# Kernel tuning notes

Measured on AMD Instinct MI355X. Metric: run time of the kernel, lower is better.

The kernel has to match this reference:

```python
import jax, jax.numpy as jnp
import numpy as np

TOP_K = 2  # num_experts_per_tok


def setup_inputs() -> dict:
    key = jax.random.key(0)
    ks = jax.random.split(key, 5)
    B, T, D, E, F = 2, 2048, 1024, 8, 2048
    scale_d = 1.0 / np.sqrt(D)
    scale_f = 1.0 / np.sqrt(F)
    return {
        "x": jax.random.normal(ks[0], (B, T, D), jnp.float32),
        "kernel_router_DE": jax.random.normal(ks[1], (D, E), jnp.float32) * scale_d,
        "kernel_gating_EDF": jax.random.normal(ks[2], (E, D, F), jnp.float32) * scale_d,
        "kernel_up_EDF": jax.random.normal(ks[3], (E, D, F), jnp.float32) * scale_d,
        "kernel_down_EFD": jax.random.normal(ks[4], (E, F, D), jnp.float32) * scale_f,
    }


def reference(x, kernel_router_DE, kernel_gating_EDF, kernel_up_EDF, kernel_down_EFD):
    E = kernel_router_DE.shape[-1]
    x = x.astype(jnp.float32)

    # --- Router: logits -> softmax -> top_k -> renormalize with softmax ---
    router_logits_BTE = jnp.einsum('BTD,DE->BTE', x, kernel_router_DE)
    probs_BTE = jax.nn.softmax(router_logits_BTE.astype(jnp.float32), axis=-1)
    weights_BTX, indices_BTX = jax.lax.top_k(probs_BTE, TOP_K)
    norm_weights_BTX = jax.nn.softmax(weights_BTX, axis=-1)

    # --- Scatter top-k weights back to dense per-expert weights ---
    one_hot_BTXE = jax.nn.one_hot(indices_BTX, num_classes=E, dtype=jnp.float32)
    full_weights_BTE = jnp.sum(one_hot_BTXE * norm_weights_BTX[..., None], axis=2)

    # --- Dense all-expert MLP (gating * up -> down), weighted combine ---
    gating_BTEF = jnp.einsum('BTD,EDF->BTEF', x, kernel_gating_EDF)
    fuse_BTEF = jax.nn.silu(gating_BTEF) * jnp.einsum('BTD,EDF->BTEF', x, kernel_up_EDF)
    down_BTED = jnp.einsum('BTEF,EFD->BTED', fuse_BTEF, kernel_down_EFD)
    out_BTD = jnp.einsum('BTED,BTE->BTD', down_BTED, full_weights_BTE)
    return out_BTD.astype(jnp.float32)
```

## Files before the change

kernel.cpp:

```cpp
#include <hip/hip_runtime.h>
#include <cstdint>

#define N_TOK 4096
#define DIM   1024
#define NEXP  8
#define FDIM  2048

typedef _Float16 f16_t;
typedef _Float16 f16x8 __attribute__((ext_vector_type(8)));
typedef float    f32x4 __attribute__((ext_vector_type(4)));

__device__ inline unsigned packh(float a, float b) {
    union { f16_t h[2]; unsigned u; } p;
    p.h[0] = (f16_t)a; p.h[1] = (f16_t)b;
    return p.u;
}

__device__ inline void gl2lds16(const void* g, void* l) {
    __builtin_amdgcn_global_load_lds(
        (const __attribute__((address_space(1))) unsigned*)g,
        (__attribute__((address_space(3))) unsigned*)l, 16, 0, 0);
}

__global__ __launch_bounds__(256) void router_kernel(
    const float* __restrict__ x, const float* __restrict__ wr,
    float* __restrict__ topw, int* __restrict__ counts, int* __restrict__ bucket)
{
    __shared__ float r[NEXP][DIM];
    __shared__ int sIdx[32];
    int tid = threadIdx.x;
    for (int i = tid; i < DIM * NEXP / 4; i += 256) {
        float4 v = ((const float4*)wr)[i];
        int base = i * 4;
        r[(base + 0) & 7][(base + 0) >> 3] = v.x;
        r[(base + 1) & 7][(base + 1) >> 3] = v.y;
        r[(base + 2) & 7][(base + 2) >> 3] = v.z;
        r[(base + 3) & 7][(base + 3) >> 3] = v.w;
    }
    __syncthreads();
    int wave = tid >> 6, lane = tid & 63;
    int t0 = blockIdx.x * 16 + wave * 4;
    for (int tt = 0; tt < 4; ++tt) {
        int t = t0 + tt;
        float acc[NEXP];
#pragma unroll
        for (int e = 0; e < NEXP; e++) acc[e] = 0.f;
        const float* xr = x + (size_t)t * DIM;
#pragma unroll
        for (int k = 0; k < DIM / 64; k++) {
            int d = lane + k * 64;
            float xv = xr[d];
#pragma unroll
            for (int e = 0; e < NEXP; e++) acc[e] += xv * r[e][d];
        }
#pragma unroll
        for (int e = 0; e < NEXP; e++) {
#pragma unroll
            for (int off = 32; off > 0; off >>= 1)
                acc[e] += __shfl_xor(acc[e], off, 64);
        }
        if (lane == 0) {
            float mx = acc[0];
#pragma unroll
            for (int e = 1; e < NEXP; e++) mx = fmaxf(mx, acc[e]);
            float p[NEXP]; float s = 0.f;
#pragma unroll
            for (int e = 0; e < NEXP; e++) { p[e] = expf(acc[e] - mx); s += p[e]; }
            float inv = 1.f / s;
#pragma unroll
            for (int e = 0; e < NEXP; e++) p[e] *= inv;
            int i1 = 0; float p1 = p[0];
#pragma unroll
            for (int e = 1; e < NEXP; e++) if (p[e] > p1) { p1 = p[e]; i1 = e; }
            int i2 = -1; float p2 = -1.f;
#pragma unroll
            for (int e = 0; e < NEXP; e++) if (e != i1 && p[e] > p2) { p2 = p[e]; i2 = e; }
            float e2 = expf(p2 - p1);
            float w1 = 1.f / (1.f + e2);
            topw[t * 2 + 0] = w1;
            topw[t * 2 + 1] = e2 * w1;
            int j = (wave * 4 + tt) * 2;
            sIdx[j + 0] = i1;
            sIdx[j + 1] = i2;
        }
    }
    __syncthreads();
    if (tid < NEXP) {
        int cnt = 0;
#pragma unroll
        for (int j = 0; j < 32; j++) cnt += (sIdx[j] == tid) ? 1 : 0;
        if (cnt > 0) {
            int pos = atomicAdd(&counts[tid * 32], cnt);
#pragma unroll
            for (int j = 0; j < 32; j++)
                if (sIdx[j] == tid)
                    bucket[tid * N_TOK + pos++] = (blockIdx.x * 16 + (j >> 1)) * 2 + (j & 1);
        }
    }
}

__global__ __launch_bounds__(256) void xcast_kernel(const float* __restrict__ x, f16_t* __restrict__ xf)
{
    int i = blockIdx.x * 256 + threadIdx.x;
    float4 a = ((const float4*)x)[2 * i];
    float4 b = ((const float4*)x)[2 * i + 1];
    union { f16_t h[8]; uint4 u; } p;
    p.h[0] = (f16_t)a.x; p.h[1] = (f16_t)a.y; p.h[2] = (f16_t)a.z; p.h[3] = (f16_t)a.w;
    p.h[4] = (f16_t)b.x; p.h[5] = (f16_t)b.y; p.h[6] = (f16_t)b.z; p.h[7] = (f16_t)b.w;
    ((uint4*)xf)[i] = p.u;
}

__global__ __launch_bounds__(256) void transpose_cvt(
    const float* __restrict__ inA, const float* __restrict__ inB,
    f16_t* __restrict__ outA, f16_t* __restrict__ outB,
    int R, int C, int tiles_r, int nA)
{
    __shared__ unsigned sP[64][68];
    int m = blockIdx.y;
    const float* in; f16_t* out;
    if (m < nA) { in = inA + (size_t)m * DIM * FDIM; out = outA + (size_t)m * DIM * FDIM; }
    else        { in = inB + (size_t)(m - nA) * DIM * FDIM; out = outB + (size_t)(m - nA) * DIM * FDIM; }
    int tix = blockIdx.x;
    int rb = (tix % tiles_r) * 128;
    int cb = (tix / tiles_r) * 64;
    int t = threadIdx.x;
    int dp = t >> 2;
    int fc = (t & 3) * 16;
    const float* r0 = in + (size_t)(rb + 2 * dp) * C + cb + fc;
    const float* r1 = r0 + C;
#pragma unroll
    for (int j = 0; j < 16; j += 4) {
        float4 a = *(const float4*)(r0 + j);
        float4 b = *(const float4*)(r1 + j);
        sP[fc + j + 0][dp] = packh(a.x, b.x);
        sP[fc + j + 1][dp] = packh(a.y, b.y);
        sP[fc + j + 2][dp] = packh(a.z, b.z);
        sP[fc + j + 3][dp] = packh(a.w, b.w);
    }
    __syncthreads();
    int c = t >> 2;
    int rc = t & 3;
    uint4* dst = (uint4*)(out + (size_t)(cb + c) * R + rb + rc * 32);
    const unsigned* src = &sP[c][rc * 16];
#pragma unroll
    for (int j = 0; j < 4; j++)
        dst[j] = *(const uint4*)(src + j * 4);
}

__global__ __launch_bounds__(256) void gateup_kernel(
    const f16_t* __restrict__ xf,
    const f16_t* __restrict__ wgT, const f16_t* __restrict__ wuT,
    const int* __restrict__ counts, const int* __restrict__ bucket,
    f16_t* __restrict__ H)
{
    int e = blockIdx.z;
    int cnt = counts[e * 32];
    int m0 = blockIdx.y * 128;
    if (m0 >= cnt) return;
    int n0 = blockIdx.x * 64;

    __shared__ f16_t sA[128 * 32];
    __shared__ f16_t sBg[64 * 32];
    __shared__ f16_t sBu[64 * 32];
    __shared__ int sEnt[128];

    int tid = threadIdx.x;
    if (tid < 128) {
        int i = m0 + tid;
        sEnt[tid] = bucket[e * N_TOK + (i < cnt ? i : m0)];
    }
    __syncthreads();

    int wave = tid >> 6, lane = tid & 63;
    int q = ((lane & 3) - (lane >> 3)) & 3;
    int rA0 = wave * 32 + (lane >> 2);
    int rA1 = rA0 + 16;
    int rB  = wave * 16 + (lane >> 2);
    const f16_t* gA0 = xf + (size_t)(sEnt[rA0] >> 1) * DIM + q * 8;
    const f16_t* gA1 = xf + (size_t)(sEnt[rA1] >> 1) * DIM + q * 8;
    const f16_t* gBg = wgT + ((size_t)e * FDIM + n0 + rB) * DIM + q * 8;
    const f16_t* gBu = wuT + ((size_t)e * FDIM + n0 + rB) * DIM + q * 8;
    f16_t* lA0 = &sA[wave * 1024 + lane * 8];
    f16_t* lA1 = lA0 + 512;
    f16_t* lBg = &sBg[wave * 512 + lane * 8];
    f16_t* lBu = &sBu[wave * 512 + lane * 8];

    f32x4 accG[4][2], accU[4][2];
    f32x4 zero = {0.f, 0.f, 0.f, 0.f};
#pragma unroll
    for (int i = 0; i < 4; i++)
#pragma unroll
        for (int j = 0; j < 2; j++) { accG[i][j] = zero; accU[i][j] = zero; }

    int wm = (wave & 1) * 64, wn = (wave >> 1) * 32;
    int fm = lane & 15, quad = lane >> 4;
    int p8 = ((quad + (fm >> 1)) & 3) * 8;

    for (int k0 = 0; k0 < DIM; k0 += 32) {
        gl2lds16(gA0 + k0, lA0);
        gl2lds16(gA1 + k0, lA1);
        gl2lds16(gBg + k0, lBg);
        gl2lds16(gBu + k0, lBu);
        __syncthreads();
        f16x8 af[4], bg[2], bu[2];
#pragma unroll
        for (int mi = 0; mi < 4; mi++)
            af[mi] = *(const f16x8*)&sA[(wm + mi * 16 + fm) * 32 + p8];
#pragma unroll
        for (int ni = 0; ni < 2; ni++) {
            bg[ni] = *(const f16x8*)&sBg[(wn + ni * 16 + fm) * 32 + p8];
            bu[ni] = *(const f16x8*)&sBu[(wn + ni * 16 + fm) * 32 + p8];
        }
#pragma unroll
        for (int mi = 0; mi < 4; mi++)
#pragma unroll
            for (int ni = 0; ni < 2; ni++) {
                accG[mi][ni] = __builtin_amdgcn_mfma_f32_16x16x32_f16(af[mi], bg[ni], accG[mi][ni], 0, 0, 0);
                accU[mi][ni] = __builtin_amdgcn_mfma_f32_16x16x32_f16(af[mi], bu[ni], accU[mi][ni], 0, 0, 0);
            }
        __syncthreads();
    }
    int crow = quad * 4, ccol = fm;
#pragma unroll
    for (int mi = 0; mi < 4; mi++) {
#pragma unroll
        for (int i = 0; i < 4; i++) {
            int m = wm + mi * 16 + crow + i;
            if (m0 + m < cnt) {
                int ent = sEnt[m];
                f16_t* hr = H + (size_t)ent * FDIM + n0 + wn;
#pragma unroll
                for (int ni = 0; ni < 2; ni++) {
                    float g = accG[mi][ni][i], u = accU[mi][ni][i];
                    float h = (g / (1.f + __expf(-g))) * u;
                    hr[ni * 16 + ccol] = (f16_t)h;
                }
            }
        }
    }
}

__global__ __launch_bounds__(256) void down_kernel(
    const f16_t* __restrict__ H, const f16_t* __restrict__ wdT,
    const int* __restrict__ counts, const int* __restrict__ bucket,
    const float* __restrict__ topw, float* __restrict__ Y)
{
    int e = blockIdx.z;
    int cnt = counts[e * 32];
    int m0 = blockIdx.y * 128;
    if (m0 >= cnt) return;
    int n0 = blockIdx.x * 128;

    __shared__ f16_t sA[128 * 32];
    __shared__ f16_t sB[128 * 32];
    __shared__ int sEnt[128];

    int tid = threadIdx.x;
    if (tid < 128) {
        int i = m0 + tid;
        sEnt[tid] = bucket[e * N_TOK + (i < cnt ? i : m0)];
    }
    __syncthreads();

    int wave = tid >> 6, lane = tid & 63;
    int q = ((lane & 3) - (lane >> 3)) & 3;
    int r0 = wave * 32 + (lane >> 2);
    int r1 = r0 + 16;
    const f16_t* gA0 = H + (size_t)sEnt[r0] * FDIM + q * 8;
    const f16_t* gA1 = H + (size_t)sEnt[r1] * FDIM + q * 8;
    const f16_t* gB0 = wdT + ((size_t)e * DIM + n0 + r0) * FDIM + q * 8;
    const f16_t* gB1 = wdT + ((size_t)e * DIM + n0 + r1) * FDIM + q * 8;
    f16_t* lA0 = &sA[wave * 1024 + lane * 8];
    f16_t* lA1 = lA0 + 512;
    f16_t* lB0 = &sB[wave * 1024 + lane * 8];
    f16_t* lB1 = lB0 + 512;

    f32x4 acc[4][4];
    f32x4 zero = {0.f, 0.f, 0.f, 0.f};
#pragma unroll
    for (int i = 0; i < 4; i++)
#pragma unroll
        for (int j = 0; j < 4; j++) acc[i][j] = zero;

    int wm = (wave & 1) * 64, wn = (wave >> 1) * 64;
    int fm = lane & 15, quad = lane >> 4;
    int p8 = ((quad + (fm >> 1)) & 3) * 8;

    for (int k0 = 0; k0 < FDIM; k0 += 32) {
        gl2lds16(gA0 + k0, lA0);
        gl2lds16(gA1 + k0, lA1);
        gl2lds16(gB0 + k0, lB0);
        gl2lds16(gB1 + k0, lB1);
        __syncthreads();
        f16x8 af[4], bf[4];
#pragma unroll
        for (int mi = 0; mi < 4; mi++)
            af[mi] = *(const f16x8*)&sA[(wm + mi * 16 + fm) * 32 + p8];
#pragma unroll
        for (int ni = 0; ni < 4; ni++)
            bf[ni] = *(const f16x8*)&sB[(wn + ni * 16 + fm) * 32 + p8];
#pragma unroll
        for (int mi = 0; mi < 4; mi++)
#pragma unroll
            for (int ni = 0; ni < 4; ni++)
                acc[mi][ni] = __builtin_amdgcn_mfma_f32_16x16x32_f16(af[mi], bf[ni], acc[mi][ni], 0, 0, 0);
        __syncthreads();
    }
    int crow = quad * 4, ccol = fm;
#pragma unroll
    for (int mi = 0; mi < 4; mi++) {
#pragma unroll
        for (int i = 0; i < 4; i++) {
            int m = wm + mi * 16 + crow + i;
            if (m0 + m < cnt) {
                int ent = sEnt[m];
                float w = topw[ent];
                float* yr = Y + (size_t)ent * DIM + n0 + wn;
#pragma unroll
                for (int ni = 0; ni < 4; ni++)
                    yr[ni * 16 + ccol] = w * acc[mi][ni][i];
            }
        }
    }
}

__global__ __launch_bounds__(256) void combine_kernel(
    const float* __restrict__ Y, float* __restrict__ out)
{
    int i = blockIdx.x * 256 + threadIdx.x;
    int t = i >> 8;
    int c = i & 255;
    float4 a = ((const float4*)Y)[(size_t)(2 * t) * 256 + c];
    float4 b = ((const float4*)Y)[(size_t)(2 * t + 1) * 256 + c];
    float4 o;
    o.x = a.x + b.x; o.y = a.y + b.y; o.z = a.z + b.z; o.w = a.w + b.w;
    ((float4*)out)[i] = o;
}

extern "C" void kernel_launch(void* const* d_in, const int* in_sizes, int n_in,
                              void* d_out, int out_size, void* d_ws, size_t ws_size,
                              hipStream_t stream) {
    const float* x  = (const float*)d_in[0];
    const float* wr = (const float*)d_in[1];
    const float* wg = (const float*)d_in[2];
    const float* wu = (const float*)d_in[3];
    const float* wd = (const float*)d_in[4];
    float* out = (float*)d_out;
    char* ws = (char*)d_ws;
    const size_t MB = 1ull << 20;

    int*   counts = (int*)ws;
    int*   bucket = (int*)(ws + 1024);
    float* topw   = (float*)(ws + 160 * 1024);
    f16_t* xf     = (f16_t*)(ws + 1 * MB);
    f16_t* wgT    = (f16_t*)(ws + 9 * MB);
    f16_t* wuT    = (f16_t*)(ws + 41 * MB);
    f16_t* H      = (f16_t*)(ws + 73 * MB);
    f16_t* wdT    = (f16_t*)(ws + 1 * MB);
    float* Y      = (float*)(ws + 33 * MB);

    hipMemsetAsync(counts, 0, 1024, stream);
    router_kernel<<<256, 256, 0, stream>>>(x, wr, topw, counts, bucket);
    xcast_kernel<<<2048, 256, 0, stream>>>(x, xf);
    transpose_cvt<<<dim3(256, 16), 256, 0, stream>>>(wg, wu, wgT, wuT, DIM, FDIM, DIM / 128, NEXP);
    gateup_kernel<<<dim3(FDIM / 64, 32, NEXP), 256, 0, stream>>>(xf, wgT, wuT, counts, bucket, H);
    transpose_cvt<<<dim3(256, 8), 256, 0, stream>>>(wd, wd, wdT, wdT, FDIM, DIM, FDIM / 128, NEXP);
    down_kernel<<<dim3(DIM / 128, 32, NEXP), 256, 0, stream>>>(H, wdT, counts, bucket, topw, Y);
    combine_kernel<<<4096, 256, 0, stream>>>(Y, out);
}
```

Baseline: 413.7 us.

## Rewrite gate/up GEMM with 256x128 tiles, double-buffered LDS and expert-interleaved scheduling

After: 463.9 us. +12.1%, slower.

```diff
diff --git a/kernel.cpp b/kernel.cpp
--- a/kernel.cpp
+++ b/kernel.cpp
@@ -20,6 +20,11 @@
     __builtin_amdgcn_global_load_lds(
         (const __attribute__((address_space(1))) unsigned*)g,
         (__attribute__((address_space(3))) unsigned*)l, 16, 0, 0);
+}
+
+template<int N>
+__device__ inline void vmw() {
+    asm volatile("s_waitcnt vmcnt(%0)" :: "i"(N) : "memory");
 }
 
 __global__ __launch_bounds__(256) void router_kernel(
@@ -147,93 +152,134 @@
         dst[j] = *(const uint4*)(src + j * 4);
 }
 
-__global__ __launch_bounds__(256) void gateup_kernel(
+#define STG_A(NB, SLOT, KO)                                                     \
+    gl2lds16(srcA0 + (KO), &lds[(NB)*32768 + (SLOT)*8192 + tid*8]);             \
+    gl2lds16(srcA1 + (KO), &lds[(NB)*32768 + (SLOT)*8192 + 4096 + tid*8])
+#define STG_B(NB, SLOT, KO)                                                     \
+    gl2lds16(srcB0 + (KO), &lds[(NB)*32768 + (SLOT)*8192 + tid*8]);             \
+    gl2lds16(srcB1 + (KO), &lds[(NB)*32768 + (SLOT)*8192 + 4096 + tid*8])
+
+#define PHASE(KS, NH, VM, STAGE_STMT)                                           \
+    {                                                                           \
+        STAGE_STMT;                                                             \
+        vmw<VM>();                                                              \
+        __builtin_amdgcn_s_barrier();                                           \
+        if ((NH) == 0) {                                                        \
+            _Pragma("unroll")                                                   \
+            for (int mi = 0; mi < 8; mi++)                                      \
+                a[mi] = *(const f16x8*)&lds[bofs + ((KS)?2:0)*8192 +            \
+                         (wr*128 + mi*16 + fm)*32 + p8];                        \
+        }                                                                       \
+        bb0 = *(const f16x8*)&lds[bofs + ((KS)?3:1)*8192 +                      \
+               (wc*64 + ((NH)*2+0)*16 + fm)*32 + p8];                           \
+        bb1 = *(const f16x8*)&lds[bofs + ((KS)?3:1)*8192 +                      \
+               (wc*64 + ((NH)*2+1)*16 + fm)*32 + p8];                           \
+        __builtin_amdgcn_s_setprio(1);                                          \
+        _Pragma("unroll")                                                       \
+        for (int mi = 0; mi < 8; mi++) {                                        \
+            acc[mi][(NH)*2+0] = __builtin_amdgcn_mfma_f32_16x16x32_f16(         \
+                a[mi], bb0, acc[mi][(NH)*2+0], 0, 0, 0);                        \
+            acc[mi][(NH)*2+1] = __builtin_amdgcn_mfma_f32_16x16x32_f16(         \
+                a[mi], bb1, acc[mi][(NH)*2+1], 0, 0, 0);                        \
+        }                                                                       \
+        __builtin_amdgcn_s_setprio(0);                                          \
+        __builtin_amdgcn_s_barrier();                                           \
+    }
+
+__global__ __launch_bounds__(512) void gateup_kernel(
     const f16_t* __restrict__ xf,
     const f16_t* __restrict__ wgT, const f16_t* __restrict__ wuT,
     const int* __restrict__ counts, const int* __restrict__ bucket,
     f16_t* __restrict__ H)
 {
-    int e = blockIdx.z;
+    int flat = blockIdx.x + (blockIdx.y << 4) + (blockIdx.z << 8);
+    int chunk = ((flat & 7) << 8) | (flat >> 3);
+    int e  = chunk >> 8;
+    int rr = chunk & 255;
+    int m0 = (rr & 15) * 256;
+    int f0 = (rr >> 4) * 128;
     int cnt = counts[e * 32];
-    int m0 = blockIdx.y * 128;
     if (m0 >= cnt) return;
-    int n0 = blockIdx.x * 64;
-
-    __shared__ f16_t sA[128 * 32];
-    __shared__ f16_t sBg[64 * 32];
-    __shared__ f16_t sBu[64 * 32];
-    __shared__ int sEnt[128];
+
+    __shared__ f16_t lds[2 * 4 * 8192];
+    __shared__ int sEnt[256];
 
     int tid = threadIdx.x;
-    if (tid < 128) {
+    if (tid < 256) {
         int i = m0 + tid;
         sEnt[tid] = bucket[e * N_TOK + (i < cnt ? i : m0)];
     }
     __syncthreads();
 
     int wave = tid >> 6, lane = tid & 63;
-    int q = ((lane & 3) - (lane >> 3)) & 3;
-    int rA0 = wave * 32 + (lane >> 2);
-    int rA1 = rA0 + 16;
-    int rB  = wave * 16 + (lane >> 2);
-    const f16_t* gA0 = xf + (size_t)(sEnt[rA0] >> 1) * DIM + q * 8;
-    const f16_t* gA1 = xf + (size_t)(sEnt[rA1] >> 1) * DIM + q * 8;
-    const f16_t* gBg = wgT + ((size_t)e * FDIM + n0 + rB) * DIM + q * 8;
-    const f16_t* gBu = wuT + ((size_t)e * FDIM + n0 + rB) * DIM + q * 8;
-    f16_t* lA0 = &sA[wave * 1024 + lane * 8];
-    f16_t* lA1 = lA0 + 512;
-    f16_t* lBg = &sBg[wave * 512 + lane * 8];
-    f16_t* lBu = &sBu[wave * 512 + lane * 8];
-
-    f32x4 accG[4][2], accU[4][2];
-    f32x4 zero = {0.f, 0.f, 0.f, 0.f};
-#pragma unroll
-    for (int i = 0; i < 4; i++)
-#pragma unroll
-        for (int j = 0; j < 2; j++) { accG[i][j] = zero; accU[i][j] = zero; }
-
-    int wm = (wave & 1) * 64, wn = (wave >> 1) * 32;
+    int wr = wave >> 2, wc = wave & 3;
     int fm = lane & 15, quad = lane >> 4;
     int p8 = ((quad + (fm >> 1)) & 3) * 8;
 
-    for (int k0 = 0; k0 < DIM; k0 += 32) {
-        gl2lds16(gA0 + k0, lA0);
-        gl2lds16(gA1 + k0, lA1);
-        gl2lds16(gBg + k0, lBg);
-        gl2lds16(gBu + k0, lBu);
-        __syncthreads();
-        f16x8 af[4], bg[2], bu[2];
-#pragma unroll
-        for (int mi = 0; mi < 4; mi++)
-            af[mi] = *(const f16x8*)&sA[(wm + mi * 16 + fm) * 32 + p8];
-#pragma unroll
-        for (int ni = 0; ni < 2; ni++) {
-            bg[ni] = *(const f16x8*)&sBg[(wn + ni * 16 + fm) * 32 + p8];
-            bu[ni] = *(const f16x8*)&sBu[(wn + ni * 16 + fm) * 32 + p8];
-        }
-#pragma unroll
-        for (int mi = 0; mi < 4; mi++)
-#pragma unroll
-            for (int ni = 0; ni < 2; ni++) {
-                accG[mi][ni] = __builtin_amdgcn_mfma_f32_16x16x32_f16(af[mi], bg[ni], accG[mi][ni], 0, 0, 0);
-                accU[mi][ni] = __builtin_amdgcn_mfma_f32_16x16x32_f16(af[mi], bu[ni], accU[mi][ni], 0, 0, 0);
-            }
-        __syncthreads();
-    }
-    int crow = quad * 4, ccol = fm;
-#pragma unroll
-    for (int mi = 0; mi < 4; mi++) {
+    int row0 = tid >> 2;
+    int row1 = 128 + row0;
+    int c0 = ((tid & 3) - (row0 >> 1)) & 3;
+    int c1 = ((tid & 3) - (row1 >> 1)) & 3;
+    const f16_t* srcA0 = xf + (size_t)(sEnt[row0] >> 1) * DIM + c0 * 8;
+    const f16_t* srcA1 = xf + (size_t)(sEnt[row1] >> 1) * DIM + c1 * 8;
+    int wc4_0 = row0 >> 6, sub0 = row0 & 63;
+    int wc4_1 = row1 >> 6, sub1 = row1 & 63;
+    const f16_t* srcB0 = ((sub0 & 32) ? wuT : wgT) +
+        ((size_t)e * FDIM + f0 + wc4_0 * 32 + (sub0 & 31)) * DIM + c0 * 8;
+    const f16_t* srcB1 = ((sub1 & 32) ? wuT : wgT) +
+        ((size_t)e * FDIM + f0 + wc4_1 * 32 + (sub1 & 31)) * DIM + c1 * 8;
+
+    f32x4 acc[8][4];
+    f32x4 zero = {0.f, 0.f, 0.f, 0.f};
+#pragma unroll
+    for (int i = 0; i < 8; i++)
+#pragma unroll
+        for (int j = 0; j < 4; j++) acc[i][j] = zero;
+
+    f16x8 a[8], bb0, bb1;
+
+    STG_A(0, 0, 0);
+    STG_B(0, 1, 0);
+    STG_A(0, 2, 32);
+    STG_B(0, 3, 32);
+    vmw<0>();
+    __builtin_amdgcn_s_barrier();
+
+    const int NT = DIM / 64;
+    int b = 0;
+    for (int t = 0; t < NT - 1; ++t) {
+        int nb = b ^ 1;
+        int bofs = b * 32768;
+        int ko = (t + 1) * 64;
+        PHASE(0, 0, 6, STG_A(nb, 0, ko));
+        PHASE(0, 1, 6, STG_B(nb, 1, ko));
+        PHASE(1, 0, 6, STG_A(nb, 2, ko + 32));
+        PHASE(1, 1, 6, STG_B(nb, 3, ko + 32));
+        b = nb;
+    }
+    {
+        int bofs = b * 32768;
+        PHASE(0, 0, 4, );
+        PHASE(0, 1, 4, );
+        PHASE(1, 0, 2, );
+        PHASE(1, 1, 0, );
+    }
+
+    int crow = quad * 4;
+#pragma unroll
+    for (int mi = 0; mi < 8; mi++) {
 #pragma unroll
         for (int i = 0; i < 4; i++) {
-            int m = wm + mi * 16 + crow + i;
-            if (m0 + m < cnt) {
-                int ent = sEnt[m];
-                f16_t* hr = H + (size_t)ent * FDIM + n0 + wn;
+            int row = wr * 128 + mi * 16 + crow + i;
+            if (m0 + row < cnt) {
+                int ent = sEnt[row];
+                f16_t* hr = H + (size_t)ent * FDIM + f0 + wc * 32;
 #pragma unroll
                 for (int ni = 0; ni < 2; ni++) {
-                    float g = accG[mi][ni][i], u = accU[mi][ni][i];
+                    float g = acc[mi][ni][i];
+                    float u = acc[mi][ni + 2][i];
                     float h = (g / (1.f + __expf(-g))) * u;
-                    hr[ni * 16 + ccol] = (f16_t)h;
+                    hr[ni * 16 + fm] = (f16_t)h;
                 }
             }
         }
@@ -363,7 +409,7 @@
     router_kernel<<<256, 256, 0, stream>>>(x, wr, topw, counts, bucket);
     xcast_kernel<<<2048, 256, 0, stream>>>(x, xf);
     transpose_cvt<<<dim3(256, 16), 256, 0, stream>>>(wg, wu, wgT, wuT, DIM, FDIM, DIM / 128, NEXP);
-    gateup_kernel<<<dim3(FDIM / 64, 32, NEXP), 256, 0, stream>>>(xf, wgT, wuT, counts, bucket, H);
+    gateup_kernel<<<dim3(16, 16, 8), 512, 0, stream>>>(xf, wgT, wuT, counts, bucket, H);
     transpose_cvt<<<dim3(256, 8), 256, 0, stream>>>(wd, wd, wdT, wdT, FDIM, DIM, FDIM / 128, NEXP);
     down_kernel<<<dim3(DIM / 128, 32, NEXP), 256, 0, stream>>>(H, wdT, counts, bucket, topw, Y);
     combine_kernel<<<4096, 256, 0, stream>>>(Y, out);
```

## Triple-buffer LDS in MoE GEMMs and fuse x cast into router

Applied to the files above, without the earlier changes.

Result: slower. 458.4 us (+10.8%).

```diff
diff --git a/kernel.cpp b/kernel.cpp
--- a/kernel.cpp
+++ b/kernel.cpp
@@ -22,13 +22,34 @@
         (__attribute__((address_space(3))) unsigned*)l, 16, 0, 0);
 }
 
+template<int N>
+__device__ inline void vmw() {
+    asm volatile("s_waitcnt vmcnt(%0)" :: "i"(N) : "memory");
+}
+
 __global__ __launch_bounds__(256) void router_kernel(
     const float* __restrict__ x, const float* __restrict__ wr,
-    float* __restrict__ topw, int* __restrict__ counts, int* __restrict__ bucket)
+    float* __restrict__ topw, int* __restrict__ counts, int* __restrict__ bucket,
+    f16_t* __restrict__ xf)
 {
     __shared__ float r[NEXP][DIM];
     __shared__ int sIdx[32];
     int tid = threadIdx.x;
+
+    {
+        const float* xblk = x + (size_t)blockIdx.x * 16 * DIM;
+        f16_t* xfblk = xf + (size_t)blockIdx.x * 16 * DIM;
+#pragma unroll
+        for (int i = tid; i < 16 * DIM / 8; i += 256) {
+            float4 a = ((const float4*)xblk)[2 * i];
+            float4 b = ((const float4*)xblk)[2 * i + 1];
+            union { f16_t h[8]; uint4 u; } pk;
+            pk.h[0] = (f16_t)a.x; pk.h[1] = (f16_t)a.y; pk.h[2] = (f16_t)a.z; pk.h[3] = (f16_t)a.w;
+            pk.h[4] = (f16_t)b.x; pk.h[5] = (f16_t)b.y; pk.h[6] = (f16_t)b.z; pk.h[7] = (f16_t)b.w;
+            ((uint4*)xfblk)[i] = pk.u;
+        }
+    }
+
     for (int i = tid; i < DIM * NEXP / 4; i += 256) {
         float4 v = ((const float4*)wr)[i];
         int base = i * 4;
@@ -97,17 +118,6 @@
                     bucket[tid * N_TOK + pos++] = (blockIdx.x * 16 + (j >> 1)) * 2 + (j & 1);
         }
     }
-}
-
-__global__ __launch_bounds__(256) void xcast_kernel(const float* __restrict__ x, f16_t* __restrict__ xf)
-{
-    int i = blockIdx.x * 256 + threadIdx.x;
-    float4 a = ((const float4*)x)[2 * i];
-    float4 b = ((const float4*)x)[2 * i + 1];
-    union { f16_t h[8]; uint4 u; } p;
-    p.h[0] = (f16_t)a.x; p.h[1] = (f16_t)a.y; p.h[2] = (f16_t)a.z; p.h[3] = (f16_t)a.w;
-    p.h[4] = (f16_t)b.x; p.h[5] = (f16_t)b.y; p.h[6] = (f16_t)b.z; p.h[7] = (f16_t)b.w;
-    ((uint4*)xf)[i] = p.u;
 }
 
 __global__ __launch_bounds__(256) void transpose_cvt(
@@ -147,6 +157,34 @@
         dst[j] = *(const uint4*)(src + j * 4);
 }
 
+#define GU_STG(B, KO)                                                           \
+    gl2lds16(gA0 + (KO), lA0 + (B) * 4096);                                     \
+    gl2lds16(gA1 + (KO), lA1 + (B) * 4096);                                     \
+    gl2lds16(gBg + (KO), lBg + (B) * 2048);                                     \
+    gl2lds16(gBu + (KO), lBu + (B) * 2048);
+
+#define GU_COMPUTE(RB)                                                          \
+    {                                                                           \
+        f16x8 af[4], bg[2], bu[2];                                              \
+        _Pragma("unroll")                                                       \
+        for (int mi = 0; mi < 4; mi++)                                          \
+            af[mi] = *(const f16x8*)&sA[(RB) * 4096 + (wm + mi * 16 + fm) * 32 + p8]; \
+        _Pragma("unroll")                                                       \
+        for (int ni = 0; ni < 2; ni++) {                                        \
+            bg[ni] = *(const f16x8*)&sBg[(RB) * 2048 + (wn + ni * 16 + fm) * 32 + p8]; \
+            bu[ni] = *(const f16x8*)&sBu[(RB) * 2048 + (wn + ni * 16 + fm) * 32 + p8]; \
+        }                                                                       \
+        __builtin_amdgcn_s_setprio(1);                                          \
+        _Pragma("unroll")                                                       \
+        for (int mi = 0; mi < 4; mi++)                                          \
+            _Pragma("unroll")                                                   \
+            for (int ni = 0; ni < 2; ni++) {                                    \
+                accG[mi][ni] = __builtin_amdgcn_mfma_f32_16x16x32_f16(af[mi], bg[ni], accG[mi][ni], 0, 0, 0); \
+                accU[mi][ni] = __builtin_amdgcn_mfma_f32_16x16x32_f16(af[mi], bu[ni], accU[mi][ni], 0, 0, 0); \
+            }                                                                   \
+        __builtin_amdgcn_s_setprio(0);                                          \
+    }
+
 __global__ __launch_bounds__(256) void gateup_kernel(
     const f16_t* __restrict__ xf,
     const f16_t* __restrict__ wgT, const f16_t* __restrict__ wuT,
@@ -159,9 +197,9 @@
     if (m0 >= cnt) return;
     int n0 = blockIdx.x * 64;
 
-    __shared__ f16_t sA[128 * 32];
-    __shared__ f16_t sBg[64 * 32];
-    __shared__ f16_t sBu[64 * 32];
+    __shared__ f16_t sA[3 * 128 * 32];
+    __shared__ f16_t sBg[3 * 64 * 32];
+    __shared__ f16_t sBu[3 * 64 * 32];
     __shared__ int sEnt[128];
 
     int tid = threadIdx.x;
@@ -196,30 +234,26 @@
     int fm = lane & 15, quad = lane >> 4;
     int p8 = ((quad + (fm >> 1)) & 3) * 8;
 
-    for (int k0 = 0; k0 < DIM; k0 += 32) {
-        gl2lds16(gA0 + k0, lA0);
-        gl2lds16(gA1 + k0, lA1);
-        gl2lds16(gBg + k0, lBg);
-        gl2lds16(gBu + k0, lBu);
-        __syncthreads();
-        f16x8 af[4], bg[2], bu[2];
-#pragma unroll
-        for (int mi = 0; mi < 4; mi++)
-            af[mi] = *(const f16x8*)&sA[(wm + mi * 16 + fm) * 32 + p8];
-#pragma unroll
-        for (int ni = 0; ni < 2; ni++) {
-            bg[ni] = *(const f16x8*)&sBg[(wn + ni * 16 + fm) * 32 + p8];
-            bu[ni] = *(const f16x8*)&sBu[(wn + ni * 16 + fm) * 32 + p8];
-        }
-#pragma unroll
-        for (int mi = 0; mi < 4; mi++)
-#pragma unroll
-            for (int ni = 0; ni < 2; ni++) {
-                accG[mi][ni] = __builtin_amdgcn_mfma_f32_16x16x32_f16(af[mi], bg[ni], accG[mi][ni], 0, 0, 0);
-                accU[mi][ni] = __builtin_amdgcn_mfma_f32_16x16x32_f16(af[mi], bu[ni], accU[mi][ni], 0, 0, 0);
-            }
-        __syncthreads();
-    }
+    GU_STG(0, 0);
+    GU_STG(1, 32);
+    vmw<4>();
+    __builtin_amdgcn_s_barrier();
+
+    int rb3 = 0, sb3 = 2;
+    for (int t = 0; t < 30; ++t) {
+        GU_STG(sb3, (t + 2) * 32);
+        GU_COMPUTE(rb3);
+        vmw<4>();
+        __builtin_amdgcn_s_barrier();
+        rb3 = (rb3 == 2) ? 0 : rb3 + 1;
+        sb3 = (sb3 == 2) ? 0 : sb3 + 1;
+    }
+    GU_COMPUTE(rb3);
+    vmw<0>();
+    __builtin_amdgcn_s_barrier();
+    rb3 = (rb3 == 2) ? 0 : rb3 + 1;
+    GU_COMPUTE(rb3);
+
     int crow = quad * 4, ccol = fm;
 #pragma unroll
     for (int mi = 0; mi < 4; mi++) {
@@ -239,6 +273,30 @@
         }
     }
 }
+
+#define DN_STG(B, KO)                                                           \
+    gl2lds16(gA0 + (KO), lA0 + (B) * 4096);                                     \
+    gl2lds16(gA1 + (KO), lA1 + (B) * 4096);                                     \
+    gl2lds16(gB0 + (KO), lB0 + (B) * 4096);                                     \
+    gl2lds16(gB1 + (KO), lB1 + (B) * 4096);
+
+#define DN_COMPUTE(RB)                                                          \
+    {                                                                           \
+        f16x8 af[4], bf[4];                                                     \
+        _Pragma("unroll")                                                       \
+        for (int mi = 0; mi < 4; mi++)                                          \
+            af[mi] = *(const f16x8*)&sA[(RB) * 4096 + (wm + mi * 16 + fm) * 32 + p8]; \
+        _Pragma("unroll")                                                       \
+        for (int ni = 0; ni < 4; ni++)                                          \
+            bf[ni] = *(const f16x8*)&sB[(RB) * 4096 + (wn + ni * 16 + fm) * 32 + p8]; \
+        __builtin_amdgcn_s_setprio(1);                                          \
+        _Pragma("unroll")                                                       \
+        for (int mi = 0; mi < 4; mi++)                                          \
+            _Pragma("unroll")                                                   \
+            for (int ni = 0; ni < 4; ni++)                                      \
+                acc[mi][ni] = __builtin_amdgcn_mfma_f32_16x16x32_f16(af[mi], bf[ni], acc[mi][ni], 0, 0, 0); \
+        __builtin_amdgcn_s_setprio(0);                                          \
+    }
 
 __global__ __launch_bounds__(256) void down_kernel(
     const f16_t* __restrict__ H, const f16_t* __restrict__ wdT,
@@ -251,8 +309,8 @@
     if (m0 >= cnt) return;
     int n0 = blockIdx.x * 128;
 
-    __shared__ f16_t sA[128 * 32];
-    __shared__ f16_t sB[128 * 32];
+    __shared__ f16_t sA[3 * 128 * 32];
+    __shared__ f16_t sB[3 * 128 * 32];
     __shared__ int sEnt[128];
 
     int tid = threadIdx.x;
@@ -286,26 +344,26 @@
     int fm = lane & 15, quad = lane >> 4;
     int p8 = ((quad + (fm >> 1)) & 3) * 8;
 
-    for (int k0 = 0; k0 < FDIM; k0 += 32) {
-        gl2lds16(gA0 + k0, lA0);
-        gl2lds16(gA1 + k0, lA1);
-        gl2lds16(gB0 + k0, lB0);
-        gl2lds16(gB1 + k0, lB1);
-        __syncthreads();
-        f16x8 af[4], bf[4];
-#pragma unroll
-        for (int mi = 0; mi < 4; mi++)
-            af[mi] = *(const f16x8*)&sA[(wm + mi * 16 + fm) * 32 + p8];
-#pragma unroll
-        for (int ni = 0; ni < 4; ni++)
-            bf[ni] = *(const f16x8*)&sB[(wn + ni * 16 + fm) * 32 + p8];
-#pragma unroll
-        for (int mi = 0; mi < 4; mi++)
-#pragma unroll
-            for (int ni = 0; ni < 4; ni++)
-                acc[mi][ni] = __builtin_amdgcn_mfma_f32_16x16x32_f16(af[mi], bf[ni], acc[mi][ni], 0, 0, 0);
-        __syncthreads();
-    }
+    DN_STG(0, 0);
+    DN_STG(1, 32);
+    vmw<4>();
+    __builtin_amdgcn_s_barrier();
+
+    int rb3 = 0, sb3 = 2;
+    for (int t = 0; t < 62; ++t) {
+        DN_STG(sb3, (t + 2) * 32);
+        DN_COMPUTE(rb3);
+        vmw<4>();
+        __builtin_amdgcn_s_barrier();
+        rb3 = (rb3 == 2) ? 0 : rb3 + 1;
+        sb3 = (sb3 == 2) ? 0 : sb3 + 1;
+    }
+    DN_COMPUTE(rb3);
+    vmw<0>();
+    __builtin_amdgcn_s_barrier();
+    rb3 = (rb3 == 2) ? 0 : rb3 + 1;
+    DN_COMPUTE(rb3);
+
     int crow = quad * 4, ccol = fm;
 #pragma unroll
     for (int mi = 0; mi < 4; mi++) {
@@ -360,8 +418,7 @@
     float* Y      = (float*)(ws + 33 * MB);
 
     hipMemsetAsync(counts, 0, 1024, stream);
-    router_kernel<<<256, 256, 0, stream>>>(x, wr, topw, counts, bucket);
-    xcast_kernel<<<2048, 256, 0, stream>>>(x, xf);
+    router_kernel<<<256, 256, 0, stream>>>(x, wr, topw, counts, bucket, xf);
     transpose_cvt<<<dim3(256, 16), 256, 0, stream>>>(wg, wu, wgT, wuT, DIM, FDIM, DIM / 128, NEXP);
     gateup_kernel<<<dim3(FDIM / 64, 32, NEXP), 256, 0, stream>>>(xf, wgT, wuT, counts, bucket, H);
     transpose_cvt<<<dim3(256, 8), 256, 0, stream>>>(wd, wd, wdT, wdT, FDIM, DIM, FDIM / 128, NEXP);
```

## Double K-tile depth in MoE GEMMs and fuse x fp16 cast into router

Applied to the files above, without the earlier changes.

Measured after the change: 428.3 us. 1.04x slower.

```diff
diff --git a/kernel.cpp b/kernel.cpp
--- a/kernel.cpp
+++ b/kernel.cpp
@@ -24,11 +24,27 @@
 
 __global__ __launch_bounds__(256) void router_kernel(
     const float* __restrict__ x, const float* __restrict__ wr,
-    float* __restrict__ topw, int* __restrict__ counts, int* __restrict__ bucket)
+    float* __restrict__ topw, int* __restrict__ counts, int* __restrict__ bucket,
+    f16_t* __restrict__ xf)
 {
     __shared__ float r[NEXP][DIM];
     __shared__ int sIdx[32];
     int tid = threadIdx.x;
+
+    {
+        const float* xblk = x + (size_t)blockIdx.x * 16 * DIM;
+        f16_t* xfblk = xf + (size_t)blockIdx.x * 16 * DIM;
+#pragma unroll
+        for (int i = tid; i < 16 * DIM / 8; i += 256) {
+            float4 a = ((const float4*)xblk)[2 * i];
+            float4 b = ((const float4*)xblk)[2 * i + 1];
+            union { f16_t h[8]; uint4 u; } pk;
+            pk.h[0] = (f16_t)a.x; pk.h[1] = (f16_t)a.y; pk.h[2] = (f16_t)a.z; pk.h[3] = (f16_t)a.w;
+            pk.h[4] = (f16_t)b.x; pk.h[5] = (f16_t)b.y; pk.h[6] = (f16_t)b.z; pk.h[7] = (f16_t)b.w;
+            ((uint4*)xfblk)[i] = pk.u;
+        }
+    }
+
     for (int i = tid; i < DIM * NEXP / 4; i += 256) {
         float4 v = ((const float4*)wr)[i];
         int base = i * 4;
@@ -97,17 +113,6 @@
                     bucket[tid * N_TOK + pos++] = (blockIdx.x * 16 + (j >> 1)) * 2 + (j & 1);
         }
     }
-}
-
-__global__ __launch_bounds__(256) void xcast_kernel(const float* __restrict__ x, f16_t* __restrict__ xf)
-{
-    int i = blockIdx.x * 256 + threadIdx.x;
-    float4 a = ((const float4*)x)[2 * i];
-    float4 b = ((const float4*)x)[2 * i + 1];
-    union { f16_t h[8]; uint4 u; } p;
-    p.h[0] = (f16_t)a.x; p.h[1] = (f16_t)a.y; p.h[2] = (f16_t)a.z; p.h[3] = (f16_t)a.w;
-    p.h[4] = (f16_t)b.x; p.h[5] = (f16_t)b.y; p.h[6] = (f16_t)b.z; p.h[7] = (f16_t)b.w;
-    ((uint4*)xf)[i] = p.u;
 }
 
 __global__ __launch_bounds__(256) void transpose_cvt(
@@ -159,9 +164,9 @@
     if (m0 >= cnt) return;
     int n0 = blockIdx.x * 64;
 
-    __shared__ f16_t sA[128 * 32];
-    __shared__ f16_t sBg[64 * 32];
-    __shared__ f16_t sBu[64 * 32];
+    __shared__ f16_t sA[128 * 64];
+    __shared__ f16_t sBg[64 * 64];
+    __shared__ f16_t sBu[64 * 64];
     __shared__ int sEnt[128];
 
     int tid = threadIdx.x;
@@ -172,18 +177,18 @@
     __syncthreads();
 
     int wave = tid >> 6, lane = tid & 63;
-    int q = ((lane & 3) - (lane >> 3)) & 3;
-    int rA0 = wave * 32 + (lane >> 2);
-    int rA1 = rA0 + 16;
-    int rB  = wave * 16 + (lane >> 2);
-    const f16_t* gA0 = xf + (size_t)(sEnt[rA0] >> 1) * DIM + q * 8;
-    const f16_t* gA1 = xf + (size_t)(sEnt[rA1] >> 1) * DIM + q * 8;
-    const f16_t* gBg = wgT + ((size_t)e * FDIM + n0 + rB) * DIM + q * 8;
-    const f16_t* gBu = wuT + ((size_t)e * FDIM + n0 + rB) * DIM + q * 8;
-    f16_t* lA0 = &sA[wave * 1024 + lane * 8];
-    f16_t* lA1 = lA0 + 512;
-    f16_t* lBg = &sBg[wave * 512 + lane * 8];
-    f16_t* lBu = &sBu[wave * 512 + lane * 8];
+    int c8 = (((tid & 7) - (tid >> 3)) & 7) * 8;
+    int ra = tid >> 3;
+
+    const f16_t* gA[4];
+#pragma unroll
+    for (int j = 0; j < 4; j++)
+        gA[j] = xf + (size_t)(sEnt[ra + j * 32] >> 1) * DIM + c8;
+    const f16_t* gBg0 = wgT + ((size_t)e * FDIM + n0 + ra) * DIM + c8;
+    const f16_t* gBu0 = wuT + ((size_t)e * FDIM + n0 + ra) * DIM + c8;
+    f16_t* dA  = &sA[tid * 8];
+    f16_t* dBg = &sBg[tid * 8];
+    f16_t* dBu = &sBu[tid * 8];
 
     f32x4 accG[4][2], accU[4][2];
     f32x4 zero = {0.f, 0.f, 0.f, 0.f};
@@ -194,30 +199,38 @@
 
     int wm = (wave & 1) * 64, wn = (wave >> 1) * 32;
     int fm = lane & 15, quad = lane >> 4;
-    int p8 = ((quad + (fm >> 1)) & 3) * 8;
-
-    for (int k0 = 0; k0 < DIM; k0 += 32) {
-        gl2lds16(gA0 + k0, lA0);
-        gl2lds16(gA1 + k0, lA1);
-        gl2lds16(gBg + k0, lBg);
-        gl2lds16(gBu + k0, lBu);
+
+    for (int k0 = 0; k0 < DIM; k0 += 64) {
+#pragma unroll
+        for (int j = 0; j < 4; j++)
+            gl2lds16(gA[j] + k0, dA + j * 2048);
+        gl2lds16(gBg0 + k0, dBg);
+        gl2lds16(gBg0 + 32 * DIM + k0, dBg + 2048);
+        gl2lds16(gBu0 + k0, dBu);
+        gl2lds16(gBu0 + 32 * DIM + k0, dBu + 2048);
         __syncthreads();
-        f16x8 af[4], bg[2], bu[2];
-#pragma unroll
-        for (int mi = 0; mi < 4; mi++)
-            af[mi] = *(const f16x8*)&sA[(wm + mi * 16 + fm) * 32 + p8];
-#pragma unroll
-        for (int ni = 0; ni < 2; ni++) {
-            bg[ni] = *(const f16x8*)&sBg[(wn + ni * 16 + fm) * 32 + p8];
-            bu[ni] = *(const f16x8*)&sBu[(wn + ni * 16 + fm) * 32 + p8];
-        }
-#pragma unroll
-        for (int mi = 0; mi < 4; mi++)
+#pragma unroll
+        for (int ks = 0; ks < 2; ++ks) {
+            f16x8 af[4], bg[2], bu[2];
+#pragma unroll
+            for (int mi = 0; mi < 4; mi++)
+                af[mi] = *(const f16x8*)&sA[(wm + mi * 16 + fm) * 64 +
+                                            ((ks * 4 + quad + fm) & 7) * 8];
 #pragma unroll
             for (int ni = 0; ni < 2; ni++) {
-                accG[mi][ni] = __builtin_amdgcn_mfma_f32_16x16x32_f16(af[mi], bg[ni], accG[mi][ni], 0, 0, 0);
-                accU[mi][ni] = __builtin_amdgcn_mfma_f32_16x16x32_f16(af[mi], bu[ni], accU[mi][ni], 0, 0, 0);
+                bg[ni] = *(const f16x8*)&sBg[(wn + ni * 16 + fm) * 64 +
+                                              ((ks * 4 + quad + fm) & 7) * 8];
+                bu[ni] = *(const f16x8*)&sBu[(wn + ni * 16 + fm) * 64 +
+                                              ((ks * 4 + quad + fm) & 7) * 8];
             }
+#pragma unroll
+            for (int mi = 0; mi < 4; mi++)
+#pragma unroll
+                for (int ni = 0; ni < 2; ni++) {
+                    accG[mi][ni] = __builtin_amdgcn_mfma_f32_16x16x32_f16(af[mi], bg[ni], accG[mi][ni], 0, 0, 0);
+                    accU[mi][ni] = __builtin_amdgcn_mfma_f32_16x16x32_f16(af[mi], bu[ni], accU[mi][ni], 0, 0, 0);
+                }
+        }
         __syncthreads();
     }
     int crow = quad * 4, ccol = fm;
@@ -251,8 +264,8 @@
     if (m0 >= cnt) return;
     int n0 = blockIdx.x * 128;
 
-    __shared__ f16_t sA[128 * 32];
-    __shared__ f16_t sB[128 * 32];
+    __shared__ f16_t sA[128 * 64];
+    __shared__ f16_t sB[128 * 64];
     __shared__ int sEnt[128];
 
     int tid = threadIdx.x;
@@ -263,17 +276,18 @@
     __syncthreads();
 
     int wave = tid >> 6, lane = tid & 63;
-    int q = ((lane & 3) - (lane >> 3)) & 3;
-    int r0 = wave * 32 + (lane >> 2);
-    int r1 = r0 + 16;
-    const f16_t* gA0 = H + (size_t)sEnt[r0] * FDIM + q * 8;
-    const f16_t* gA1 = H + (size_t)sEnt[r1] * FDIM + q * 8;
-    const f16_t* gB0 = wdT + ((size_t)e * DIM + n0 + r0) * FDIM + q * 8;
-    const f16_t* gB1 = wdT + ((size_t)e * DIM + n0 + r1) * FDIM + q * 8;
-    f16_t* lA0 = &sA[wave * 1024 + lane * 8];
-    f16_t* lA1 = lA0 + 512;
-    f16_t* lB0 = &sB[wave * 1024 + lane * 8];
-    f16_t* lB1 = lB0 + 512;
+    int c8 = (((tid & 7) - (tid >> 3)) & 7) * 8;
+    int ra = tid >> 3;
+
+    const f16_t* gA[4];
+    const f16_t* gB[4];
+#pragma unroll
+    for (int j = 0; j < 4; j++) {
+        gA[j] = H + (size_t)sEnt[ra + j * 32] * FDIM + c8;
+        gB[j] = wdT + ((size_t)e * DIM + n0 + ra + j * 32) * FDIM + c8;
+    }
+    f16_t* dA = &sA[tid * 8];
+    f16_t* dB = &sB[tid * 8];
 
     f32x4 acc[4][4];
     f32x4 zero = {0.f, 0.f, 0.f, 0.f};
@@ -284,26 +298,31 @@
 
     int wm = (wave & 1) * 64, wn = (wave >> 1) * 64;
     int fm = lane & 15, quad = lane >> 4;
-    int p8 = ((quad + (fm >> 1)) & 3) * 8;
-
-    for (int k0 = 0; k0 < FDIM; k0 += 32) {
-        gl2lds16(gA0 + k0, lA0);
-        gl2lds16(gA1 + k0, lA1);
-        gl2lds16(gB0 + k0, lB0);
-        gl2lds16(gB1 + k0, lB1);
+
+    for (int k0 = 0; k0 < FDIM; k0 += 64) {
+#pragma unroll
+        for (int j = 0; j < 4; j++) {
+            gl2lds16(gA[j] + k0, dA + j * 2048);
+            gl2lds16(gB[j] + k0, dB + j * 2048);
+        }
         __syncthreads();
-        f16x8 af[4], bf[4];
-#pragma unroll
-        for (int mi = 0; mi < 4; mi++)
-            af[mi] = *(const f16x8*)&sA[(wm + mi * 16 + fm) * 32 + p8];
-#pragma unroll
-        for (int ni = 0; ni < 4; ni++)
-            bf[ni] = *(const f16x8*)&sB[(wn + ni * 16 + fm) * 32 + p8];
-#pragma unroll
-        for (int mi = 0; mi < 4; mi++)
+#pragma unroll
+        for (int ks = 0; ks < 2; ++ks) {
+            f16x8 af[4], bf[4];
+#pragma unroll
+            for (int mi = 0; mi < 4; mi++)
+                af[mi] = *(const f16x8*)&sA[(wm + mi * 16 + fm) * 64 +
+                                            ((ks * 4 + quad + fm) & 7) * 8];
 #pragma unroll
             for (int ni = 0; ni < 4; ni++)
-                acc[mi][ni] = __builtin_amdgcn_mfma_f32_16x16x32_f16(af[mi], bf[ni], acc[mi][ni], 0, 0, 0);
+                bf[ni] = *(const f16x8*)&sB[(wn + ni * 16 + fm) * 64 +
+                                            ((ks * 4 + quad + fm) & 7) * 8];
+#pragma unroll
+            for (int mi = 0; mi < 4; mi++)
+#pragma unroll
+                for (int ni = 0; ni < 4; ni++)
+                    acc[mi][ni] = __builtin_amdgcn_mfma_f32_16x16x32_f16(af[mi], bf[ni], acc[mi][ni], 0, 0, 0);
+        }
         __syncthreads();
     }
     int crow = quad * 4, ccol = fm;
@@ -360,8 +379,7 @@
     float* Y      = (float*)(ws + 33 * MB);
 
     hipMemsetAsync(counts, 0, 1024, stream);
-    router_kernel<<<256, 256, 0, stream>>>(x, wr, topw, counts, bucket);
-    xcast_kernel<<<2048, 256, 0, stream>>>(x, xf);
+    router_kernel<<<256, 256, 0, stream>>>(x, wr, topw, counts, bucket, xf);
     transpose_cvt<<<dim3(256, 16), 256, 0, stream>>>(wg, wu, wgT, wuT, DIM, FDIM, DIM / 128, NEXP);
     gateup_kernel<<<dim3(FDIM / 64, 32, NEXP), 256, 0, stream>>>(xf, wgT, wuT, counts, bucket, H);
     transpose_cvt<<<dim3(256, 8), 256, 0, stream>>>(wd, wd, wdT, wdT, FDIM, DIM, FDIM / 128, NEXP);
```
